# Performance work log

Hardware: AMD Instinct MI355X
Metric: run time of the kernel (lower is better)

## Reference

```python
import jax, jax.numpy as jnp
import numpy as np

B, S, D, H = 8, 1024, 1024, 16
HD = D // H  # head dim 64
NUM_REL = 7


def setup_inputs() -> dict:
    key = jax.random.key(0)
    ks = jax.random.split(key, 10)
    s = 0.02
    return {
        "hidden_states": jax.random.normal(ks[0], (B, S, D), dtype=jnp.float32),
        "attention_mask": jnp.zeros((B, 1, 1, S), dtype=jnp.float32),
        "relation": jax.random.randint(ks[1], (B, S, S), 0, NUM_REL, dtype=jnp.int32),
        "Wq": jax.random.normal(ks[2], (D, D), dtype=jnp.float32) * s,
        "bq": jnp.zeros((D,), dtype=jnp.float32),
        "Wk": jax.random.normal(ks[3], (D, D), dtype=jnp.float32) * s,
        "bk": jnp.zeros((D,), dtype=jnp.float32),
        "Wv": jax.random.normal(ks[4], (D, D), dtype=jnp.float32) * s,
        "bv": jnp.zeros((D,), dtype=jnp.float32),
        "rel_emb": jax.random.normal(ks[5], (NUM_REL, H), dtype=jnp.float32) * s,
    }


def reference(hidden_states, attention_mask, relation, Wq, bq, Wk, bk, Wv, bv, rel_emb):
    def heads(x):  # [B,S,D] -> [B,H,S,HD]
        return x.reshape(B, S, H, HD).transpose(0, 2, 1, 3)

    q = heads(hidden_states @ Wq.T + bq)
    k = heads(hidden_states @ Wk.T + bk)
    v = heads(hidden_states @ Wv.T + bv)

    scores = jnp.einsum("bhqd,bhkd->bhqk", q, k) / jnp.sqrt(jnp.float32(HD))
    # relation bias: gather [B,S,S,H] then move H to dim 1
    rel_bias = rel_emb[relation].transpose(0, 3, 1, 2)  # [B,H,S,S]
    scores = scores + rel_bias + attention_mask
    probs = jax.nn.softmax(scores, axis=-1)  # dropout is identity in eval
    ctx = jnp.einsum("bhqk,bhkd->bhqd", probs, v)
    return ctx.transpose(0, 2, 1, 3).reshape(B, S, D)
```

## Files before the change

kernel.cpp:

```cpp
#include <hip/hip_runtime.h>

#define NB 8
#define NS 1024
#define ND 1024
#define NH 16
#define NHD 64

typedef __attribute__((ext_vector_type(8))) short bf16x8;
typedef __attribute__((ext_vector_type(4))) float f32x4;

#define GLOAD_LDS16(g, l) __builtin_amdgcn_global_load_lds(                    \
    (const __attribute__((address_space(1))) void*)(g),                        \
    (__attribute__((address_space(3))) void*)(l), 16, 0, 0)

static __device__ __forceinline__ unsigned short f2bf(float f) {
    unsigned int u = __builtin_bit_cast(unsigned int, f);
    unsigned int r = u + 0x7fffu + ((u >> 16) & 1u);
    return (unsigned short)(r >> 16);
}

static __device__ __forceinline__ unsigned int cvtpk(float lo, float hi) {
    unsigned int r;
    asm("v_cvt_pk_bf16_f32 %0, %1, %2" : "=v"(r) : "v"(lo), "v"(hi));
    return r;
}

__global__ void cvt_f32_bf16(const float* __restrict__ in, unsigned short* __restrict__ out, int n) {
    int i = (blockIdx.x * blockDim.x + threadIdx.x) * 4;
    if (i >= n) return;
    float4 v = *reinterpret_cast<const float4*>(in + i);
    ushort4 o;
    o.x = f2bf(v.x); o.y = f2bf(v.y); o.z = f2bf(v.z); o.w = f2bf(v.w);
    *reinterpret_cast<ushort4*>(out + i) = o;
}

__global__ __launch_bounds__(256) void qkv_gemm(
    const unsigned short* __restrict__ A,
    const unsigned short* __restrict__ Wq, const unsigned short* __restrict__ Wk,
    const unsigned short* __restrict__ Wv,
    const float* __restrict__ bq, const float* __restrict__ bk, const float* __restrict__ bv,
    unsigned short* __restrict__ Qo, unsigned short* __restrict__ Ko, unsigned short* __restrict__ Vo)
{
    const int z = blockIdx.z;
    const unsigned short* W = (z == 0) ? Wq : (z == 1) ? Wk : Wv;
    const float* bias = (z == 0) ? bq : (z == 1) ? bk : bv;
    const int m0 = blockIdx.x * 128;
    const int n0 = blockIdx.y * 128;

    __shared__ unsigned short As[128][64];
    __shared__ unsigned short Bs[128][64];

    const int tid = threadIdx.x;
    const int lane = tid & 63;
    const int wave = tid >> 6;
    const int wm = wave >> 1, wn = wave & 1;

    f32x4 acc[4][4] = {};

    const int crow = lane >> 3;
    const int gcol = ((lane & 7) ^ crow) * 8;
    const int kofs = (lane >> 4) * 8;

    for (int kb = 0; kb < ND; kb += 64) {
#pragma unroll
        for (int cc = 0; cc < 4; ++cc) {
            int c = wave * 4 + cc;
            GLOAD_LDS16(&A[(size_t)(m0 + c * 8 + crow) * ND + kb + gcol], &As[c * 8][0]);
            GLOAD_LDS16(&W[(size_t)(n0 + c * 8 + crow) * ND + kb + gcol], &Bs[c * 8][0]);
        }
        __syncthreads();
#pragma unroll
        for (int kk = 0; kk < 2; ++kk) {
            const int colx = (kk * 32 + kofs) ^ ((lane & 7) * 8);
            bf16x8 af[4], bfr[4];
#pragma unroll
            for (int i = 0; i < 4; ++i) {
                af[i]  = *reinterpret_cast<const bf16x8*>(&As[wm * 64 + i * 16 + (lane & 15)][colx]);
                bfr[i] = *reinterpret_cast<const bf16x8*>(&Bs[wn * 64 + i * 16 + (lane & 15)][colx]);
            }
#pragma unroll
            for (int mi = 0; mi < 4; ++mi)
#pragma unroll
                for (int ni = 0; ni < 4; ++ni)
                    acc[mi][ni] = __builtin_amdgcn_mfma_f32_16x16x32_bf16(af[mi], bfr[ni], acc[mi][ni], 0, 0, 0);
        }
        __syncthreads();
    }

#pragma unroll
    for (int ni = 0; ni < 4; ++ni) {
        int n = n0 + wn * 64 + ni * 16 + (lane & 15);
        float bv_ = bias[n];
        int h = n >> 6, hd = n & 63;
#pragma unroll
        for (int mi = 0; mi < 4; ++mi) {
            int m = m0 + wm * 64 + mi * 16 + (lane >> 4) * 4;
            int b = m >> 10, s = m & 1023;
            if (z == 2) {
                ushort4 o;
                o.x = f2bf(acc[mi][ni][0] + bv_);
                o.y = f2bf(acc[mi][ni][1] + bv_);
                o.z = f2bf(acc[mi][ni][2] + bv_);
                o.w = f2bf(acc[mi][ni][3] + bv_);
                *reinterpret_cast<ushort4*>(&Vo[(((size_t)b * NH + h) * NHD + hd) * NS + s]) = o;
            } else {
                unsigned short* O = (z == 0) ? Qo : Ko;
#pragma unroll
                for (int r2 = 0; r2 < 4; ++r2)
                    O[(((size_t)b * NH + h) * NS + s + r2) * NHD + hd] = f2bf(acc[mi][ni][r2] + bv_);
            }
        }
    }
}

__global__ __launch_bounds__(512) void flash_attn(
    const unsigned short* __restrict__ Q, const unsigned short* __restrict__ Kb,
    const unsigned short* __restrict__ Vt,
    const int* __restrict__ rel, const float* __restrict__ rel_emb,
    const float* __restrict__ mask, float* __restrict__ out)
{
    const int q0 = blockIdx.x * 128;
    const int h = blockIdx.y;
    const int b = blockIdx.z;
    const int tid = threadIdx.x, lane = tid & 63, wave = tid >> 6;
    const int g = lane >> 4, l15 = lane & 15;

    __shared__ unsigned short Ks[2][64][64];
    __shared__ unsigned short Vs[2][64][64];
    __shared__ unsigned short Ps[8][16][64];
    __shared__ float s_re2[8];
    const float LOG2E = 1.4426950408889634f;
    const float SCL2 = 0.125f * 1.4426950408889634f;
    if (tid < 7) s_re2[tid] = rel_emb[tid * NH + h] * LOG2E;

    const unsigned short* Qh = Q  + (((size_t)b * NH + h) * NS) * NHD;
    const unsigned short* Kh = Kb + (((size_t)b * NH + h) * NS) * NHD;
    const unsigned short* Vh = Vt + (((size_t)b * NH + h) * NHD) * NS;
    const int qg = q0 + wave * 16 + l15;
    const int* __restrict__ relrow = rel + (size_t)b * NS * NS + (size_t)qg * NS;
    const float* __restrict__ maskb = mask + (size_t)b * NS;

    bf16x8 qa[2];
    qa[0] = *reinterpret_cast<const bf16x8*>(&Qh[(size_t)qg * NHD + g * 8]);
    qa[1] = *reinterpret_cast<const bf16x8*>(&Qh[(size_t)qg * NHD + 32 + g * 8]);

    f32x4 ctx[4] = {};
    float m2 = 4.0f, l_run = 0.f;

    const int crow = lane >> 3;
    const int gcol = ((lane & 7) ^ crow) * 8;
    const int swz8 = (lane & 7) * 8;

#define STAGE(buf, kv)                                                                          \
    {                                                                                           \
        GLOAD_LDS16(&Kh[(size_t)((kv) + wave * 8 + crow) * NHD + gcol], &Ks[buf][wave * 8][0]); \
        GLOAD_LDS16(&Vh[(size_t)(wave * 8 + crow) * NS + (kv) + gcol], &Vs[buf][wave * 8][0]);  \
    }

    STAGE(0, 0);
    __syncthreads();

    for (int t = 0; t < 16; ++t) {
        const int cur = t & 1;
        const int kv0 = t * 64;

        int4 rc4[4];
        float4 mv4[4];
#pragma unroll
        for (int nt = 0; nt < 4; ++nt) {
            rc4[nt] = *reinterpret_cast<const int4*>(&relrow[kv0 + nt * 16 + 4 * g]);
            mv4[nt] = *reinterpret_cast<const float4*>(&maskb[kv0 + nt * 16 + 4 * g]);
        }
        if (t < 15) STAGE(cur ^ 1, kv0 + 64);

        f32x4 sc[4] = {};
        __builtin_amdgcn_s_setprio(1);
#pragma unroll
        for (int kk = 0; kk < 2; ++kk) {
            const int colx = (kk * 32 + g * 8) ^ swz8;
#pragma unroll
            for (int nt = 0; nt < 4; ++nt) {
                bf16x8 kfrag = *reinterpret_cast<const bf16x8*>(&Ks[cur][nt * 16 + l15][colx]);
                sc[nt] = __builtin_amdgcn_mfma_f32_16x16x32_bf16(kfrag, qa[kk], sc[nt], 0, 0, 0);
            }
        }
        __builtin_amdgcn_s_setprio(0);

        float pmax = -1e30f;
#pragma unroll
        for (int nt = 0; nt < 4; ++nt) {
            const int rca[4] = {rc4[nt].x, rc4[nt].y, rc4[nt].z, rc4[nt].w};
            const float mva[4] = {mv4[nt].x, mv4[nt].y, mv4[nt].z, mv4[nt].w};
#pragma unroll
            for (int r = 0; r < 4; ++r) {
                float bias2 = fmaf(mva[r], LOG2E, s_re2[rca[r]]);
                float v = fmaf(sc[nt][r], SCL2, bias2);
                sc[nt][r] = v;
                pmax = fmaxf(pmax, v);
            }
        }

        if (!__all(pmax - m2 <= 8.0f)) {
            float pm = fmaxf(pmax, __shfl_xor(pmax, 16));
            pm = fmaxf(pm, __shfl_xor(pm, 32));
            float mnew = fmaxf(m2, pm);
            float alpha = exp2f(m2 - mnew);
            m2 = mnew;
            l_run *= alpha;
            float ar[4];
#pragma unroll
            for (int r = 0; r < 4; ++r) ar[r] = __shfl(alpha, 4 * g + r);
#pragma unroll
            for (int ht = 0; ht < 4; ++ht)
#pragma unroll
                for (int r = 0; r < 4; ++r) ctx[ht][r] *= ar[r];
        }

#pragma unroll
        for (int nt = 0; nt < 4; ++nt) {
            float p0 = exp2f(sc[nt][0] - m2);
            float p1 = exp2f(sc[nt][1] - m2);
            float p2 = exp2f(sc[nt][2] - m2);
            float p3 = exp2f(sc[nt][3] - m2);
            l_run += (p0 + p1) + (p2 + p3);
            int pc = (2 * nt + (g >> 1)) ^ (l15 & 7);
            *reinterpret_cast<uint2*>(&Ps[wave][l15][pc * 8 + 4 * (g & 1)]) =
                make_uint2(cvtpk(p0, p1), cvtpk(p2, p3));
        }

        __builtin_amdgcn_s_setprio(1);
#pragma unroll
        for (int kk = 0; kk < 2; ++kk) {
            bf16x8 pa = *reinterpret_cast<const bf16x8*>(
                &Ps[wave][l15][((kk * 4 + g) ^ (l15 & 7)) * 8]);
            const int colx = (kk * 32 + g * 8) ^ swz8;
#pragma unroll
            for (int ht = 0; ht < 4; ++ht) {
                bf16x8 bfrag = *reinterpret_cast<const bf16x8*>(&Vs[cur][ht * 16 + l15][colx]);
                ctx[ht] = __builtin_amdgcn_mfma_f32_16x16x32_bf16(pa, bfrag, ctx[ht], 0, 0, 0);
            }
        }
        __builtin_amdgcn_s_setprio(0);
        __syncthreads();
    }
#undef STAGE

    l_run += __shfl_xor(l_run, 16);
    l_run += __shfl_xor(l_run, 32);
    float linv[4];
#pragma unroll
    for (int r = 0; r < 4; ++r) linv[r] = 1.0f / __shfl(l_run, 4 * g + r);
#pragma unroll
    for (int ht = 0; ht < 4; ++ht) {
        int hd = ht * 16 + l15;
#pragma unroll
        for (int r = 0; r < 4; ++r) {
            int qo = q0 + wave * 16 + 4 * g + r;
            out[((size_t)b * NS + qo) * ND + h * NHD + hd] = ctx[ht][r] * linv[r];
        }
    }
}

extern "C" void kernel_launch(void* const* d_in, const int* in_sizes, int n_in,
                              void* d_out, int out_size, void* d_ws, size_t ws_size,
                              hipStream_t stream) {
    const float* hs      = (const float*)d_in[0];
    const float* mask    = (const float*)d_in[1];
    const int*   rel     = (const int*)d_in[2];
    const float* Wq      = (const float*)d_in[3];
    const float* bq      = (const float*)d_in[4];
    const float* Wk      = (const float*)d_in[5];
    const float* bk      = (const float*)d_in[6];
    const float* Wv      = (const float*)d_in[7];
    const float* bv      = (const float*)d_in[8];
    const float* rel_emb = (const float*)d_in[9];
    float* out = (float*)d_out;

    char* ws = (char*)d_ws;
    unsigned short* q_bf  = (unsigned short*)(ws);
    unsigned short* k_bf  = (unsigned short*)(ws + ((size_t)16 << 20));
    unsigned short* vt_bf = (unsigned short*)(ws + ((size_t)32 << 20));
    unsigned short* hs_bf = (unsigned short*)(ws + ((size_t)48 << 20));
    unsigned short* w_bf  = (unsigned short*)(ws + ((size_t)64 << 20));

    const int nhs = NB * NS * ND;
    const int nw  = ND * ND;
    cvt_f32_bf16<<<nhs / 4 / 256, 256, 0, stream>>>(hs, hs_bf, nhs);
    cvt_f32_bf16<<<nw / 4 / 256, 256, 0, stream>>>(Wq, w_bf, nw);
    cvt_f32_bf16<<<nw / 4 / 256, 256, 0, stream>>>(Wk, w_bf + (size_t)nw, nw);
    cvt_f32_bf16<<<nw / 4 / 256, 256, 0, stream>>>(Wv, w_bf + (size_t)2 * nw, nw);

    qkv_gemm<<<dim3((NB * NS) / 128, ND / 128, 3), 256, 0, stream>>>(
        hs_bf, w_bf, w_bf + (size_t)nw, w_bf + (size_t)2 * nw,
        bq, bk, bv, q_bf, k_bf, vt_bf);

    flash_attn<<<dim3(NS / 128, NH, NB), 512, 0, stream>>>(
        q_bf, k_bf, vt_bf, rel, rel_emb, mask, out);
}
```

Measured before the change: 179.8 us.

## Permute K rows so P stays in registers, removing LDS round-trip

The K tile rows are loaded into LDS in a permuted key order, so the S accumulator layout from the QK^T MFMA lines up with the A-operand fragment layout of the PV MFMA. P is then packed to bf16 and fed straight from registers, and the per-wave Ps shared buffer with its stores and reloads is dropped. The relation and mask loads are reindexed to match the permuted key columns. This saves LDS traffic and shared memory but depends on the permutation exactly matching the MFMA fragment layouts.

Result: no change. 178.6 us (-0.6%).

```diff
diff --git a/kernel.cpp b/kernel.cpp
--- a/kernel.cpp
+++ b/kernel.cpp
@@ -8,6 +8,7 @@
 
 typedef __attribute__((ext_vector_type(8))) short bf16x8;
 typedef __attribute__((ext_vector_type(4))) float f32x4;
+typedef __attribute__((ext_vector_type(4))) unsigned int u32x4;
 
 #define GLOAD_LDS16(g, l) __builtin_amdgcn_global_load_lds(                    \
     (const __attribute__((address_space(1))) void*)(g),                        \
@@ -127,7 +128,6 @@
 
     __shared__ unsigned short Ks[2][64][64];
     __shared__ unsigned short Vs[2][64][64];
-    __shared__ unsigned short Ps[8][16][64];
     __shared__ float s_re2[8];
     const float LOG2E = 1.4426950408889634f;
     const float SCL2 = 0.125f * 1.4426950408889634f;
@@ -151,10 +151,14 @@
     const int gcol = ((lane & 7) ^ crow) * 8;
     const int swz8 = (lane & 7) * 8;
 
-#define STAGE(buf, kv)                                                                          \
-    {                                                                                           \
-        GLOAD_LDS16(&Kh[(size_t)((kv) + wave * 8 + crow) * NHD + gcol], &Ks[buf][wave * 8][0]); \
-        GLOAD_LDS16(&Vh[(size_t)(wave * 8 + crow) * NS + (kv) + gcol], &Vs[buf][wave * 8][0]);  \
+    const int rho = wave * 8 + crow;
+    const int kvperm = ((rho >> 5) << 5) + (((rho >> 2) & 3) << 3)
+                     + (((rho >> 4) & 1) << 2) + (rho & 3);
+
+#define STAGE(buf, kv)                                                                       \
+    {                                                                                        \
+        GLOAD_LDS16(&Kh[(size_t)((kv) + kvperm) * NHD + gcol], &Ks[buf][wave * 8][0]);       \
+        GLOAD_LDS16(&Vh[(size_t)(wave * 8 + crow) * NS + (kv) + gcol], &Vs[buf][wave * 8][0]); \
     }
 
     STAGE(0, 0);
@@ -167,9 +171,10 @@
         int4 rc4[4];
         float4 mv4[4];
 #pragma unroll
-        for (int nt = 0; nt < 4; ++nt) {
-            rc4[nt] = *reinterpret_cast<const int4*>(&relrow[kv0 + nt * 16 + 4 * g]);
-            mv4[nt] = *reinterpret_cast<const float4*>(&maskb[kv0 + nt * 16 + 4 * g]);
+        for (int tt = 0; tt < 4; ++tt) {
+            const int kvb = kv0 + ((tt >> 1) << 5) + 8 * g + ((tt & 1) << 2);
+            rc4[tt] = *reinterpret_cast<const int4*>(&relrow[kvb]);
+            mv4[tt] = *reinterpret_cast<const float4*>(&maskb[kvb]);
         }
         if (t < 15) STAGE(cur ^ 1, kv0 + 64);
 
@@ -179,23 +184,23 @@
         for (int kk = 0; kk < 2; ++kk) {
             const int colx = (kk * 32 + g * 8) ^ swz8;
 #pragma unroll
-            for (int nt = 0; nt < 4; ++nt) {
-                bf16x8 kfrag = *reinterpret_cast<const bf16x8*>(&Ks[cur][nt * 16 + l15][colx]);
-                sc[nt] = __builtin_amdgcn_mfma_f32_16x16x32_bf16(kfrag, qa[kk], sc[nt], 0, 0, 0);
+            for (int tt = 0; tt < 4; ++tt) {
+                bf16x8 kfrag = *reinterpret_cast<const bf16x8*>(&Ks[cur][tt * 16 + l15][colx]);
+                sc[tt] = __builtin_amdgcn_mfma_f32_16x16x32_bf16(kfrag, qa[kk], sc[tt], 0, 0, 0);
             }
         }
         __builtin_amdgcn_s_setprio(0);
 
         float pmax = -1e30f;
 #pragma unroll
-        for (int nt = 0; nt < 4; ++nt) {
-            const int rca[4] = {rc4[nt].x, rc4[nt].y, rc4[nt].z, rc4[nt].w};
-            const float mva[4] = {mv4[nt].x, mv4[nt].y, mv4[nt].z, mv4[nt].w};
+        for (int tt = 0; tt < 4; ++tt) {
+            const int rca[4] = {rc4[tt].x, rc4[tt].y, rc4[tt].z, rc4[tt].w};
+            const float mva[4] = {mv4[tt].x, mv4[tt].y, mv4[tt].z, mv4[tt].w};
 #pragma unroll
             for (int r = 0; r < 4; ++r) {
                 float bias2 = fmaf(mva[r], LOG2E, s_re2[rca[r]]);
-                float v = fmaf(sc[nt][r], SCL2, bias2);
-                sc[nt][r] = v;
+                float v = fmaf(sc[tt][r], SCL2, bias2);
+                sc[tt][r] = v;
                 pmax = fmaxf(pmax, v);
             }
         }
@@ -216,23 +221,23 @@
                 for (int r = 0; r < 4; ++r) ctx[ht][r] *= ar[r];
         }
 
-#pragma unroll
-        for (int nt = 0; nt < 4; ++nt) {
-            float p0 = exp2f(sc[nt][0] - m2);
-            float p1 = exp2f(sc[nt][1] - m2);
-            float p2 = exp2f(sc[nt][2] - m2);
-            float p3 = exp2f(sc[nt][3] - m2);
+        unsigned int pw[4][2];
+#pragma unroll
+        for (int tt = 0; tt < 4; ++tt) {
+            float p0 = exp2f(sc[tt][0] - m2);
+            float p1 = exp2f(sc[tt][1] - m2);
+            float p2 = exp2f(sc[tt][2] - m2);
+            float p3 = exp2f(sc[tt][3] - m2);
             l_run += (p0 + p1) + (p2 + p3);
-            int pc = (2 * nt + (g >> 1)) ^ (l15 & 7);
-            *reinterpret_cast<uint2*>(&Ps[wave][l15][pc * 8 + 4 * (g & 1)]) =
-                make_uint2(cvtpk(p0, p1), cvtpk(p2, p3));
+            pw[tt][0] = cvtpk(p0, p1);
+            pw[tt][1] = cvtpk(p2, p3);
         }
 
         __builtin_amdgcn_s_setprio(1);
 #pragma unroll
         for (int kk = 0; kk < 2; ++kk) {
-            bf16x8 pa = *reinterpret_cast<const bf16x8*>(
-                &Ps[wave][l15][((kk * 4 + g) ^ (l15 & 7)) * 8]);
+            u32x4 paw = {pw[2 * kk][0], pw[2 * kk][1], pw[2 * kk + 1][0], pw[2 * kk + 1][1]};
+            bf16x8 pa = __builtin_bit_cast(bf16x8, paw);
             const int colx = (kk * 32 + g * 8) ^ swz8;
 #pragma unroll
             for (int ht = 0; ht < 4; ++ht) {
```

## Keep softmax probabilities in registers via permuted K rows and MFMA row-sum

Applied to the files above, without the earlier changes.

Permutes the K rows staged into LDS so the S=QK^T accumulator layout matches the MFMA A-operand layout. The probabilities can then be packed straight into registers for the PV MFMA, and the per-wave LDS P buffer round trip goes away. The row-sum is computed with an extra MFMA against a ones vector, which replaces the shuffle reductions. The mask is cached in LDS, and relation loads are double-buffered one tile ahead with a two-step unrolled loop. A constant offset folded into the bias lets exp skip the max subtraction until the first rescale, at the cost of extra register pressure and more complex control flow.

Result: faster. 172.0 us (-4.3%).

```diff
diff --git a/kernel.cpp b/kernel.cpp
--- a/kernel.cpp
+++ b/kernel.cpp
@@ -8,6 +8,7 @@
 
 typedef __attribute__((ext_vector_type(8))) short bf16x8;
 typedef __attribute__((ext_vector_type(4))) float f32x4;
+typedef __attribute__((ext_vector_type(4))) unsigned int u32x4;
 
 #define GLOAD_LDS16(g, l) __builtin_amdgcn_global_load_lds(                    \
     (const __attribute__((address_space(1))) void*)(g),                        \
@@ -127,11 +128,11 @@
 
     __shared__ unsigned short Ks[2][64][64];
     __shared__ unsigned short Vs[2][64][64];
-    __shared__ unsigned short Ps[8][16][64];
+    __shared__ float s_mask[NS];
     __shared__ float s_re2[8];
     const float LOG2E = 1.4426950408889634f;
     const float SCL2 = 0.125f * 1.4426950408889634f;
-    if (tid < 7) s_re2[tid] = rel_emb[tid * NH + h] * LOG2E;
+    if (tid < 7) s_re2[tid] = rel_emb[tid * NH + h] * LOG2E - 4.0f;
 
     const unsigned short* Qh = Q  + (((size_t)b * NH + h) * NS) * NHD;
     const unsigned short* Kh = Kb + (((size_t)b * NH + h) * NS) * NHD;
@@ -144,112 +145,135 @@
     qa[0] = *reinterpret_cast<const bf16x8*>(&Qh[(size_t)qg * NHD + g * 8]);
     qa[1] = *reinterpret_cast<const bf16x8*>(&Qh[(size_t)qg * NHD + 32 + g * 8]);
 
+    bf16x8 vone;
+#pragma unroll
+    for (int i = 0; i < 8; ++i) vone[i] = (short)0x3F80;
+
     f32x4 ctx[4] = {};
-    float m2 = 4.0f, l_run = 0.f;
+    f32x4 l_acc = {};
+    float mofs = 0.f;
+    bool everscaled = false;
 
     const int crow = lane >> 3;
     const int gcol = ((lane & 7) ^ crow) * 8;
     const int swz8 = (lane & 7) * 8;
 
+    const int rho = wave * 8 + crow;
+    const int kvperm = ((rho >> 5) << 5) + (((rho >> 2) & 3) << 3)
+                     + (((rho >> 4) & 1) << 2) + (rho & 3);
+
 #define STAGE(buf, kv)                                                                          \
     {                                                                                           \
-        GLOAD_LDS16(&Kh[(size_t)((kv) + wave * 8 + crow) * NHD + gcol], &Ks[buf][wave * 8][0]); \
+        GLOAD_LDS16(&Kh[(size_t)((kv) + kvperm) * NHD + gcol], &Ks[buf][wave * 8][0]);          \
         GLOAD_LDS16(&Vh[(size_t)(wave * 8 + crow) * NS + (kv) + gcol], &Vs[buf][wave * 8][0]);  \
     }
 
-    STAGE(0, 0);
+#define LOADRM(S, t0)                                                           \
+    {                                                                           \
+        rc##S[0] = *reinterpret_cast<const int4*>(&relrow[(t0) * 64 + 8 * g]);      \
+        rc##S[1] = *reinterpret_cast<const int4*>(&relrow[(t0) * 64 + 8 * g + 4]);  \
+        rc##S[2] = *reinterpret_cast<const int4*>(&relrow[(t0) * 64 + 8 * g + 32]); \
+        rc##S[3] = *reinterpret_cast<const int4*>(&relrow[(t0) * 64 + 8 * g + 36]); \
+    }
+
+    int4 rcA[4], rcB[4];
+
+    LOADRM(A, 0)
+    STAGE(0, 0)
+    s_mask[tid] = maskb[tid] * LOG2E;
+    s_mask[tid + 512] = maskb[tid + 512] * LOG2E;
     __syncthreads();
 
-    for (int t = 0; t < 16; ++t) {
-        const int cur = t & 1;
-        const int kv0 = t * 64;
-
-        int4 rc4[4];
-        float4 mv4[4];
-#pragma unroll
-        for (int nt = 0; nt < 4; ++nt) {
-            rc4[nt] = *reinterpret_cast<const int4*>(&relrow[kv0 + nt * 16 + 4 * g]);
-            mv4[nt] = *reinterpret_cast<const float4*>(&maskb[kv0 + nt * 16 + 4 * g]);
-        }
-        if (t < 15) STAGE(cur ^ 1, kv0 + 64);
-
-        f32x4 sc[4] = {};
-        __builtin_amdgcn_s_setprio(1);
-#pragma unroll
-        for (int kk = 0; kk < 2; ++kk) {
-            const int colx = (kk * 32 + g * 8) ^ swz8;
-#pragma unroll
-            for (int nt = 0; nt < 4; ++nt) {
-                bf16x8 kfrag = *reinterpret_cast<const bf16x8*>(&Ks[cur][nt * 16 + l15][colx]);
-                sc[nt] = __builtin_amdgcn_mfma_f32_16x16x32_bf16(kfrag, qa[kk], sc[nt], 0, 0, 0);
-            }
-        }
-        __builtin_amdgcn_s_setprio(0);
-
-        float pmax = -1e30f;
-#pragma unroll
-        for (int nt = 0; nt < 4; ++nt) {
-            const int rca[4] = {rc4[nt].x, rc4[nt].y, rc4[nt].z, rc4[nt].w};
-            const float mva[4] = {mv4[nt].x, mv4[nt].y, mv4[nt].z, mv4[nt].w};
-#pragma unroll
-            for (int r = 0; r < 4; ++r) {
-                float bias2 = fmaf(mva[r], LOG2E, s_re2[rca[r]]);
-                float v = fmaf(sc[nt][r], SCL2, bias2);
-                sc[nt][r] = v;
-                pmax = fmaxf(pmax, v);
-            }
-        }
-
-        if (!__all(pmax - m2 <= 8.0f)) {
-            float pm = fmaxf(pmax, __shfl_xor(pmax, 16));
-            pm = fmaxf(pm, __shfl_xor(pm, 32));
-            float mnew = fmaxf(m2, pm);
-            float alpha = exp2f(m2 - mnew);
-            m2 = mnew;
-            l_run *= alpha;
-            float ar[4];
-#pragma unroll
-            for (int r = 0; r < 4; ++r) ar[r] = __shfl(alpha, 4 * g + r);
-#pragma unroll
-            for (int ht = 0; ht < 4; ++ht)
-#pragma unroll
-                for (int r = 0; r < 4; ++r) ctx[ht][r] *= ar[r];
-        }
-
-#pragma unroll
-        for (int nt = 0; nt < 4; ++nt) {
-            float p0 = exp2f(sc[nt][0] - m2);
-            float p1 = exp2f(sc[nt][1] - m2);
-            float p2 = exp2f(sc[nt][2] - m2);
-            float p3 = exp2f(sc[nt][3] - m2);
-            l_run += (p0 + p1) + (p2 + p3);
-            int pc = (2 * nt + (g >> 1)) ^ (l15 & 7);
-            *reinterpret_cast<uint2*>(&Ps[wave][l15][pc * 8 + 4 * (g & 1)]) =
-                make_uint2(cvtpk(p0, p1), cvtpk(p2, p3));
-        }
-
-        __builtin_amdgcn_s_setprio(1);
-#pragma unroll
-        for (int kk = 0; kk < 2; ++kk) {
-            bf16x8 pa = *reinterpret_cast<const bf16x8*>(
-                &Ps[wave][l15][((kk * 4 + g) ^ (l15 & 7)) * 8]);
-            const int colx = (kk * 32 + g * 8) ^ swz8;
-#pragma unroll
-            for (int ht = 0; ht < 4; ++ht) {
-                bf16x8 bfrag = *reinterpret_cast<const bf16x8*>(&Vs[cur][ht * 16 + l15][colx]);
-                ctx[ht] = __builtin_amdgcn_mfma_f32_16x16x32_bf16(pa, bfrag, ctx[ht], 0, 0, 0);
-            }
-        }
-        __builtin_amdgcn_s_setprio(0);
-        __syncthreads();
-    }
+#define BODY(cur, S, SN, tc, tn)                                               \
+  {                                                                            \
+    if ((tn) < 16) {                                                           \
+      LOADRM(SN, tn)                                                           \
+      STAGE(cur ^ 1, (tn) * 64)                                                \
+    }                                                                          \
+    f32x4 sc[4] = {};                                                          \
+    __builtin_amdgcn_s_setprio(1);                                             \
+    _Pragma("unroll")                                                          \
+    for (int kk = 0; kk < 2; ++kk) {                                           \
+      const int colx = (kk * 32 + g * 8) ^ swz8;                               \
+      _Pragma("unroll")                                                        \
+      for (int tt = 0; tt < 4; ++tt) {                                         \
+        bf16x8 kfrag = *reinterpret_cast<const bf16x8*>(&Ks[cur][tt * 16 + l15][colx]); \
+        sc[tt] = __builtin_amdgcn_mfma_f32_16x16x32_bf16(kfrag, qa[kk], sc[tt], 0, 0, 0); \
+      }                                                                        \
+    }                                                                          \
+    __builtin_amdgcn_s_setprio(0);                                             \
+    float pmax = -1e30f;                                                       \
+    _Pragma("unroll")                                                          \
+    for (int tt = 0; tt < 4; ++tt) {                                           \
+      float4 mv = *reinterpret_cast<const float4*>(                            \
+          &s_mask[(tc) * 64 + ((tt >> 1) << 5) + 8 * g + ((tt & 1) << 2)]);    \
+      const int rca[4] = {rc##S[tt].x, rc##S[tt].y, rc##S[tt].z, rc##S[tt].w}; \
+      float v0 = fmaf(sc[tt][0], SCL2, s_re2[rca[0]] + mv.x);                  \
+      float v1 = fmaf(sc[tt][1], SCL2, s_re2[rca[1]] + mv.y);                  \
+      float v2 = fmaf(sc[tt][2], SCL2, s_re2[rca[2]] + mv.z);                  \
+      float v3 = fmaf(sc[tt][3], SCL2, s_re2[rca[3]] + mv.w);                  \
+      sc[tt][0] = v0; sc[tt][1] = v1; sc[tt][2] = v2; sc[tt][3] = v3;          \
+      pmax = fmaxf(pmax, fmaxf(fmaxf(v0, v1), fmaxf(v2, v3)));                 \
+    }                                                                          \
+    if (!__all(pmax <= mofs + 8.0f)) {                                         \
+      float pm = fmaxf(pmax, __shfl_xor(pmax, 16));                            \
+      pm = fmaxf(pm, __shfl_xor(pm, 32));                                      \
+      float mnew = fmaxf(mofs, pm);                                            \
+      float alpha = exp2f(mofs - mnew);                                        \
+      mofs = mnew;                                                             \
+      everscaled = true;                                                       \
+      float ar[4];                                                             \
+      _Pragma("unroll")                                                        \
+      for (int r = 0; r < 4; ++r) ar[r] = __shfl(alpha, 4 * g + r);            \
+      _Pragma("unroll")                                                        \
+      for (int r = 0; r < 4; ++r) l_acc[r] *= ar[r];                           \
+      _Pragma("unroll")                                                        \
+      for (int ht = 0; ht < 4; ++ht)                                           \
+        _Pragma("unroll")                                                      \
+        for (int r = 0; r < 4; ++r) ctx[ht][r] *= ar[r];                       \
+    }                                                                          \
+    unsigned int pw[8];                                                        \
+    if (!everscaled) {                                                         \
+      _Pragma("unroll")                                                        \
+      for (int tt = 0; tt < 4; ++tt) {                                         \
+        pw[2 * tt]     = cvtpk(exp2f(sc[tt][0]), exp2f(sc[tt][1]));            \
+        pw[2 * tt + 1] = cvtpk(exp2f(sc[tt][2]), exp2f(sc[tt][3]));            \
+      }                                                                        \
+    } else {                                                                   \
+      _Pragma("unroll")                                                        \
+      for (int tt = 0; tt < 4; ++tt) {                                         \
+        pw[2 * tt]     = cvtpk(exp2f(sc[tt][0] - mofs), exp2f(sc[tt][1] - mofs)); \
+        pw[2 * tt + 1] = cvtpk(exp2f(sc[tt][2] - mofs), exp2f(sc[tt][3] - mofs)); \
+      }                                                                        \
+    }                                                                          \
+    __builtin_amdgcn_s_setprio(1);                                             \
+    _Pragma("unroll")                                                          \
+    for (int kk = 0; kk < 2; ++kk) {                                           \
+      u32x4 paw = {pw[4 * kk], pw[4 * kk + 1], pw[4 * kk + 2], pw[4 * kk + 3]};\
+      bf16x8 pa = __builtin_bit_cast(bf16x8, paw);                             \
+      const int colx = (kk * 32 + g * 8) ^ swz8;                               \
+      l_acc = __builtin_amdgcn_mfma_f32_16x16x32_bf16(pa, vone, l_acc, 0, 0, 0); \
+      _Pragma("unroll")                                                        \
+      for (int ht = 0; ht < 4; ++ht) {                                         \
+        bf16x8 bfrag = *reinterpret_cast<const bf16x8*>(&Vs[cur][ht * 16 + l15][colx]); \
+        ctx[ht] = __builtin_amdgcn_mfma_f32_16x16x32_bf16(pa, bfrag, ctx[ht], 0, 0, 0); \
+      }                                                                        \
+    }                                                                          \
+    __builtin_amdgcn_s_setprio(0);                                             \
+    __syncthreads();                                                           \
+  }
+
+    for (int t = 0; t < 16; t += 2) {
+        BODY(0, A, B, t, t + 1)
+        BODY(1, B, A, t + 1, t + 2)
+    }
+#undef BODY
+#undef LOADRM
 #undef STAGE
 
-    l_run += __shfl_xor(l_run, 16);
-    l_run += __shfl_xor(l_run, 32);
     float linv[4];
 #pragma unroll
-    for (int r = 0; r < 4; ++r) linv[r] = 1.0f / __shfl(l_run, 4 * g + r);
+    for (int r = 0; r < 4; ++r) linv[r] = 1.0f / l_acc[r];
 #pragma unroll
     for (int ht = 0; ht < 4; ++ht) {
         int hd = ht * 16 + l15;
```
